# Performance work log

Measured on AMD Instinct MI355X. Metric: run time of the kernel, lower is better.

## Reference

```python
import jax, jax.numpy as jnp
import numpy as np

B, T, C = 4, 2048, 1024
H = 16
DH = C // H  # 64


def setup_inputs() -> dict:
    key = jax.random.key(0)
    ks = jax.random.split(key, 6)
    s = 1.0 / np.sqrt(C)
    x = jax.random.normal(ks[0], (B, T, C), dtype=jnp.float32)
    # per-head projection weights, stacked: (H, C, DH)
    Wq = jax.random.uniform(ks[1], (H, C, DH), dtype=jnp.float32, minval=-s, maxval=s)
    Wk = jax.random.uniform(ks[2], (H, C, DH), dtype=jnp.float32, minval=-s, maxval=s)
    Wv = jax.random.uniform(ks[3], (H, C, DH), dtype=jnp.float32, minval=-s, maxval=s)
    # output projection (torch Linear: y = x @ W.T + b); store as (C, C) for x @ Wo
    Wo = jax.random.uniform(ks[4], (C, C), dtype=jnp.float32, minval=-s, maxval=s)
    bo = jax.random.uniform(ks[5], (C,), dtype=jnp.float32, minval=-s, maxval=s)
    return {"x": x, "Wq": Wq, "Wk": Wk, "Wv": Wv, "Wo": Wo, "bo": bo}


def reference(x, Wq, Wk, Wv, Wo, bo):
    # x: (B,T,C) -> q,k,v: (B,H,T,DH)
    q = jnp.einsum('btc,hcd->bhtd', x, Wq)
    k = jnp.einsum('btc,hcd->bhtd', x, Wk)
    v = jnp.einsum('btc,hcd->bhtd', x, Wv)
    scale = DH ** -0.5
    scores = jnp.einsum('bhtd,bhsd->bhts', q, k) * scale  # (B,H,T,T)
    causal = jnp.tril(jnp.ones((T, T), dtype=bool))
    scores = jnp.where(causal, scores, -jnp.inf)
    wei = jax.nn.softmax(scores, axis=-1)
    out = jnp.einsum('bhts,bhsd->bhtd', wei, v)  # (B,H,T,DH)
    # concat heads: (B,T,H*DH) = (B,T,C)
    out = out.transpose(0, 2, 1, 3).reshape(B, T, C)
    return out @ Wo + bo
```

## Files before the change

kernel.cpp:

```cpp
#include <hip/hip_runtime.h>

#define T_SEQ 2048
#define C_DIM 1024
#define H_NUM 16
#define DHD   64
#define B_NUM 4
#define M_ROWS (B_NUM*T_SEQ)

typedef __bf16 bf16x8 __attribute__((ext_vector_type(8)));
typedef float  f32x4  __attribute__((ext_vector_type(4)));
typedef unsigned short ushort8 __attribute__((ext_vector_type(8)));
typedef unsigned short ushort4e __attribute__((ext_vector_type(4)));

__device__ __forceinline__ unsigned short f2b(float f){
  return __builtin_bit_cast(unsigned short, (__bf16)f);
}
__device__ __forceinline__ bf16x8 as_bf(ushort8 u){ return __builtin_bit_cast(bf16x8, u); }
__device__ __forceinline__ float exp2fast(float x){ return __builtin_amdgcn_exp2f(x); }

__device__ __forceinline__ void gload16(const void* g, void* l){
  __builtin_amdgcn_global_load_lds(
      (const __attribute__((address_space(1))) void*)g,
      (__attribute__((address_space(3))) void*)l, 16, 0, 0);
}

#define MF(a,b,c) __builtin_amdgcn_mfma_f32_16x16x32_bf16(a,b,c,0,0,0)

__global__ __launch_bounds__(256) void k_prep(const float* __restrict__ x,
                                              const float* __restrict__ wq,
                                              const float* __restrict__ wk,
                                              const float* __restrict__ wv,
                                              const float* __restrict__ wo,
                                              unsigned short* __restrict__ xb,
                                              unsigned short* __restrict__ wt,
                                              unsigned short* __restrict__ wot){
  const int bid = blockIdx.x;
  const int tid = threadIdx.x;
  if (bid < 8192){
    int i = bid*256 + tid;
    float4 f = ((const float4*)x)[i];
    ushort4e o;
    o[0]=f2b(f.x); o[1]=f2b(f.y); o[2]=f2b(f.z); o[3]=f2b(f.w);
    ((ushort4e*)xb)[i] = o;
    return;
  }
  __shared__ __align__(16) unsigned short vr[64][72];
  const int tb = bid - 8192;
  const float* S; int LS; unsigned short* D; int R0, C0; float scale = 1.f;
  if (tb < 768){
    int m = tb >> 8, rem = tb & 255;
    int h = rem >> 4, c0 = rem & 15;
    S = ((m==0)?wq:(m==1)?wk:wv) + (size_t)(h*16 + c0)*64*64;
    LS = 64;
    D = wt; R0 = m*1024 + h*64; C0 = c0*64;
    if (m == 0) scale = 0.125f * 1.4426950408889634f;
  } else {
    int tb2 = tb - 768;
    int nb = tb2 >> 4, cb = tb2 & 15;
    S = wo + (size_t)(cb*64)*1024 + nb*64;
    LS = 1024;
    D = wot; R0 = nb*64; C0 = cb*64;
  }
  #pragma unroll
  for (int i = 0; i < 2; i++){
    int id2 = tid + i*256;
    int r = id2 >> 3, e8 = (id2 & 7)*8;
    float4 a = *(const float4*)&S[(size_t)r*LS + e8];
    float4 b2 = *(const float4*)&S[(size_t)r*LS + e8 + 4];
    ushort8 u;
    u[0]=f2b(a.x*scale); u[1]=f2b(a.y*scale); u[2]=f2b(a.z*scale); u[3]=f2b(a.w*scale);
    u[4]=f2b(b2.x*scale); u[5]=f2b(b2.y*scale); u[6]=f2b(b2.z*scale); u[7]=f2b(b2.w*scale);
    *(ushort8*)&vr[r][e8 ^ ((r >> 3) << 3)] = u;
  }
  __syncthreads();
  #pragma unroll
  for (int i = 0; i < 2; i++){
    int id2 = tid + i*256;
    int d = id2 >> 3, oc = id2 & 7;
    ushort8 u;
    #pragma unroll
    for (int j = 0; j < 8; j++)
      u[j] = vr[oc*8 + j][d ^ (oc << 3)];
    *(ushort8*)&D[(size_t)(R0 + d)*1024 + C0 + oc*8] = u;
  }
}

__global__ __launch_bounds__(256) void k_gemm_qkv(const unsigned short* __restrict__ xb,
                                                  const unsigned short* __restrict__ wt,
                                                  unsigned short* __restrict__ qo,
                                                  unsigned short* __restrict__ ko,
                                                  unsigned short* __restrict__ vtr){
  __shared__ __align__(16) unsigned short smem[2][128*64];
  const int tid = threadIdx.x, lane = tid & 63, wid = tid >> 6;
  const int g = lane >> 4, tl = lane & 15;
  const int wr = wid >> 1, wc = wid & 1;
  const int id = blockIdx.x;
  const int xcd = id & 7, i = id >> 3;
  const int xm = xcd >> 1, xn = xcd & 1;
  const int mbase = (xm*16 + i/12) * 128, nbase = (xn*12 + i%12) * 128;
  const int sel = nbase >> 10;
  f32x4 acc[4][4] = {};
  if (sel < 2){
    for (int kk = 0; kk < C_DIM; kk += 64){
      __syncthreads();
      #pragma unroll
      for (int i2 = 0; i2 < 4; i2++){
        const int brow = (wid*4 + i2)*8;
        const int row  = brow + (lane >> 3);
        const int jj   = (lane & 7) ^ (row & 7);
        gload16(&xb[(size_t)(mbase+row)*C_DIM + kk + jj*8], &smem[0][brow*64]);
        gload16(&wt[(size_t)(nbase+row)*C_DIM + kk + jj*8], &smem[1][brow*64]);
      }
      __syncthreads();
      bf16x8 aF[4][2], bF[4][2];
      #pragma unroll
      for (int mb = 0; mb < 4; mb++){
        const int row = wr*64 + mb*16 + tl; const int s7 = row & 7;
        aF[mb][0] = as_bf(*(const ushort8*)&smem[0][row*64 + ((g     ^ s7)*8)]);
        aF[mb][1] = as_bf(*(const ushort8*)&smem[0][row*64 + (((4+g) ^ s7)*8)]);
      }
      #pragma unroll
      for (int nb = 0; nb < 4; nb++){
        const int row = wc*64 + nb*16 + tl; const int s7 = row & 7;
        bF[nb][0] = as_bf(*(const ushort8*)&smem[1][row*64 + ((g     ^ s7)*8)]);
        bF[nb][1] = as_bf(*(const ushort8*)&smem[1][row*64 + (((4+g) ^ s7)*8)]);
      }
      #pragma unroll
      for (int mb = 0; mb < 4; mb++)
        #pragma unroll
        for (int nb = 0; nb < 4; nb++){
          acc[mb][nb] = MF(bF[nb][0], aF[mb][0], acc[mb][nb]);
          acc[mb][nb] = MF(bF[nb][1], aF[mb][1], acc[mb][nb]);
        }
    }
    unsigned short* dst0 = (sel == 0) ? qo : ko;
    const int nloc = (nbase & 1023) + wc*64;
    #pragma unroll
    for (int mb = 0; mb < 4; mb++){
      const int t = mbase + wr*64 + mb*16 + tl;
      const int b = t >> 11, tt = t & 2047;
      #pragma unroll
      for (int nb = 0; nb < 4; nb++){
        const int nw = nloc + nb*16 + g*4;
        const int h = nw >> 6, d0 = nw & 63;
        ushort4e pk;
        #pragma unroll
        for (int r = 0; r < 4; r++) pk[r] = f2b(acc[mb][nb][r]);
        *(ushort4e*)&dst0[(((size_t)(b*H_NUM + h))*T_SEQ + tt)*DHD + d0] = pk;
      }
    }
  } else {
    for (int kk = 0; kk < C_DIM; kk += 64){
      __syncthreads();
      #pragma unroll
      for (int i2 = 0; i2 < 4; i2++){
        const int brow = (wid*4 + i2)*8;
        const int row  = brow + (lane >> 3);
        const int jj   = (lane & 7) ^ (row & 7);
        gload16(&xb[(size_t)(mbase+row)*C_DIM + kk + jj*8], &smem[0][brow*64]);
        gload16(&wt[(size_t)(nbase+row)*C_DIM + kk + jj*8], &smem[1][brow*64]);
      }
      __syncthreads();
      bf16x8 aF[4][2], bF[4][2];
      #pragma unroll
      for (int mb = 0; mb < 4; mb++){
        const int row = wr*64 + mb*16 + tl; const int s7 = row & 7;
        aF[mb][0] = as_bf(*(const ushort8*)&smem[0][row*64 + ((g     ^ s7)*8)]);
        aF[mb][1] = as_bf(*(const ushort8*)&smem[0][row*64 + (((4+g) ^ s7)*8)]);
      }
      #pragma unroll
      for (int nb = 0; nb < 4; nb++){
        const int row = wc*64 + nb*16 + tl; const int s7 = row & 7;
        bF[nb][0] = as_bf(*(const ushort8*)&smem[1][row*64 + ((g     ^ s7)*8)]);
        bF[nb][1] = as_bf(*(const ushort8*)&smem[1][row*64 + (((4+g) ^ s7)*8)]);
      }
      #pragma unroll
      for (int mb = 0; mb < 4; mb++)
        #pragma unroll
        for (int nb = 0; nb < 4; nb++){
          acc[mb][nb] = MF(aF[mb][0], bF[nb][0], acc[mb][nb]);
          acc[mb][nb] = MF(aF[mb][1], bF[nb][1], acc[mb][nb]);
        }
    }
    __syncthreads();
    unsigned short* tr = &smem[0][0];
    #pragma unroll
    for (int mb = 0; mb < 4; mb++){
      #pragma unroll
      for (int nb = 0; nb < 4; nb++){
        const int n = wc*64 + nb*16 + tl;
        const int m0 = wr*64 + mb*16 + g*4;
        ushort4e pk;
        #pragma unroll
        for (int r = 0; r < 4; r++) pk[r] = f2b(acc[mb][nb][r]);
        *(ushort4e*)&tr[n*128 + (m0 ^ ((n & 15) << 3))] = pk;
      }
    }
    __syncthreads();
    const int hbase = (nbase - 2048) >> 6;
    const int b = mbase >> 11, tloc = mbase & 2047;
    const int n = tid >> 1, half = tid & 1;
    unsigned short* vdst = vtr + (((size_t)(b*H_NUM + hbase + (n >> 6)))*DHD + (n & 63))*T_SEQ
                           + tloc + half*64;
    const int nx = (n & 15) << 3;
    #pragma unroll
    for (int c8 = 0; c8 < 8; c8++){
      const int t0 = half*64 + (c8 >> 2)*32 + (c8 & 3)*4;
      ushort4e lo = *(const ushort4e*)&tr[n*128 + ((t0     ) ^ nx)];
      ushort4e hi = *(const ushort4e*)&tr[n*128 + ((t0 + 16) ^ nx)];
      ushort8 u;
      #pragma unroll
      for (int e = 0; e < 4; e++){ u[e] = lo[e]; u[4+e] = hi[e]; }
      *(ushort8*)&vdst[c8*8] = u;
    }
  }
}

__global__ __launch_bounds__(512) void k_flash(const unsigned short* __restrict__ q,
                                               const unsigned short* __restrict__ k,
                                               const unsigned short* __restrict__ vtg,
                                               unsigned short* __restrict__ o){
  __shared__ __align__(16) unsigned short kbufs[2][128*64];
  __shared__ __align__(16) unsigned short vbufs[2][64*128];
  const int tid = threadIdx.x, lane = tid & 63, w = tid >> 6;
  const int g = lane >> 4, tl = lane & 15;
  const int id = blockIdx.x;
  const int kslot = id >> 3;
  const int bh = (id & 7)*8 + (kslot & 7);
  const int qsel = kslot >> 3;
  const int qt = (qsel < 4) ? qsel : (11 - qsel);
  const int b = bh >> 4, h = bh & 15;
  const unsigned short* qb = q   + (size_t)bh * T_SEQ * DHD;
  const unsigned short* kb = k   + (size_t)bh * T_SEQ * DHD;
  const unsigned short* vb = vtg + (size_t)bh * (size_t)DHD * T_SEQ;
  const int lrow = lane >> 3, lj = lane & 7;
  const int s7 = tl & 7;
  const int vre = lane >> 4;
  const int vh  = (lane >> 3) & 1;
  const int vcc = lane & 7;

  const int tbase = qt * 256;
  const int trow0 = tbase + w * 32;
  const int tmax = trow0 + 31;
  bf16x8 qF[2][2];
  #pragma unroll
  for (int tf = 0; tf < 2; tf++)
    #pragma unroll
    for (int ks = 0; ks < 2; ks++)
      qF[tf][ks] = as_bf(*(const ushort8*)&qb[(size_t)(trow0 + tf*16 + tl)*DHD + ks*32 + g*8]);
  f32x4 acc[2][4] = {};
  float mreg[2] = {-1e30f, -1e30f}, lreg[2] = {0.f, 0.f};
  const int nkt = 2*qt + 2;
  #pragma unroll
  for (int i = 0; i < 2; i++){
    const int krow = i*64 + w*8 + lrow;
    const int kjj  = lj ^ (krow & 7);
    gload16(&kb[(size_t)krow*DHD + kjj*8], &kbufs[0][(i*64 + w*8)*64]);
    const int vrow = i*32 + w*4 + vre;
    const int vjj  = vcc ^ (vrow & 7);
    gload16(&vb[(size_t)vrow*T_SEQ + vh*64 + vjj*8], &vbufs[0][(i*32 + w*4)*128]);
  }
  __syncthreads();
  for (int kti = 0; kti < nkt; ++kti){
    const int cur = kti & 1;
    const int kbase = kti * 128;
    if (kti + 1 < nkt){
      const int kb2 = kbase + 128;
      #pragma unroll
      for (int i = 0; i < 2; i++){
        const int krow = i*64 + w*8 + lrow;
        const int kjj  = lj ^ (krow & 7);
        gload16(&kb[(size_t)(kb2+krow)*DHD + kjj*8], &kbufs[cur^1][(i*64 + w*8)*64]);
        const int vrow = i*32 + w*4 + vre;
        const int vjj  = vcc ^ (vrow & 7);
        gload16(&vb[(size_t)vrow*T_SEQ + kb2 + vh*64 + vjj*8], &vbufs[cur^1][(i*32 + w*4)*128]);
      }
    }
    if (kbase <= tmax){
      const unsigned short* kcur = kbufs[cur];
      const unsigned short* vcur = vbufs[cur];
      f32x4 st[2][8] = {};
      __builtin_amdgcn_s_setprio(1);
      #pragma unroll
      for (int sf = 0; sf < 8; sf++){
        const int row = sf*16 + tl;
        const int r7 = row & 7;
        bf16x8 kf0 = as_bf(*(const ushort8*)&kcur[row*64 + ((g     ^ r7)*8)]);
        bf16x8 kf1 = as_bf(*(const ushort8*)&kcur[row*64 + (((4+g) ^ r7)*8)]);
        #pragma unroll
        for (int tf = 0; tf < 2; tf++){
          st[tf][sf] = MF(kf0, qF[tf][0], st[tf][sf]);
          st[tf][sf] = MF(kf1, qF[tf][1], st[tf][sf]);
        }
      }
      __builtin_amdgcn_s_setprio(0);
      if (kbase + 127 > trow0){
        #pragma unroll
        for (int tf = 0; tf < 2; tf++){
          int tg = trow0 + tf*16 + tl;
          #pragma unroll
          for (int sf = 0; sf < 8; sf++)
            #pragma unroll
            for (int r = 0; r < 4; r++)
              if (kbase + sf*16 + g*4 + r > tg) st[tf][sf][r] = -1e30f;
        }
      }
      bf16x8 pa[2][4];
      #pragma unroll
      for (int tf = 0; tf < 2; tf++){
        float mloc = -1e30f;
        #pragma unroll
        for (int sf = 0; sf < 8; sf++)
          #pragma unroll
          for (int r = 0; r < 4; r++) mloc = fmaxf(mloc, st[tf][sf][r]);
        if (__any(mloc > mreg[tf] + 8.f)){
          float mrow = fmaxf(mloc, __shfl_xor(mloc, 16));
          mrow = fmaxf(mrow, __shfl_xor(mrow, 32));
          float mnew = fmaxf(mreg[tf], mrow);
          float alpha = exp2fast(mreg[tf] - mnew);
          mreg[tf] = mnew;
          lreg[tf] *= alpha;
          #pragma unroll
          for (int df = 0; df < 4; df++)
            #pragma unroll
            for (int r = 0; r < 4; r++) acc[tf][df][r] *= alpha;
        }
        float sum = 0.f;
        #pragma unroll
        for (int q4 = 0; q4 < 4; q4++){
          ushort8 uu;
          #pragma unroll
          for (int r = 0; r < 4; r++){
            float p0 = exp2fast(st[tf][2*q4  ][r] - mreg[tf]);
            float p1 = exp2fast(st[tf][2*q4+1][r] - mreg[tf]);
            sum += p0 + p1;
            uu[r]   = f2b(p0);
            uu[4+r] = f2b(p1);
          }
          pa[tf][q4] = as_bf(uu);
        }
        lreg[tf] += sum;
      }
      __builtin_amdgcn_s_setprio(1);
      #pragma unroll
      for (int df = 0; df < 4; df++){
        const int row = df*16 + tl;
        bf16x8 vfr[4];
        #pragma unroll
        for (int q4 = 0; q4 < 4; q4++)
          vfr[q4] = as_bf(*(const ushort8*)&vcur[row*128 + (q4 >> 1)*64 + (((4*(q4 & 1) + g) ^ s7)*8)]);
        #pragma unroll
        for (int tf = 0; tf < 2; tf++)
          #pragma unroll
          for (int q4 = 0; q4 < 4; q4++)
            acc[tf][df] = MF(vfr[q4], pa[tf][q4], acc[tf][df]);
      }
      __builtin_amdgcn_s_setprio(0);
    }
    __syncthreads();
  }
  #pragma unroll
  for (int tf = 0; tf < 2; tf++){
    float l = lreg[tf];
    l += __shfl_xor(l, 16);
    l += __shfl_xor(l, 32);
    float inv = 1.f / l;
    int tg = trow0 + tf*16 + tl;
    #pragma unroll
    for (int df = 0; df < 4; df++){
      ushort4e ov;
      #pragma unroll
      for (int r = 0; r < 4; r++) ov[r] = f2b(acc[tf][df][r] * inv);
      *(ushort4e*)&o[((size_t)(b*T_SEQ + tg))*C_DIM + h*DHD + df*16 + g*4] = ov;
    }
  }
}

__global__ __launch_bounds__(256) void k_gemm_proj(const unsigned short* __restrict__ ab,
                                                   const unsigned short* __restrict__ wot,
                                                   const float* __restrict__ bo,
                                                   float* __restrict__ out){
  __shared__ __align__(16) unsigned short a_lds[128*64];
  __shared__ __align__(16) unsigned short b_lds[128*64];
  const int tid = threadIdx.x, lane = tid & 63, wid = tid >> 6;
  const int g = lane >> 4, tl = lane & 15;
  const int wr = wid >> 1, wc = wid & 1;
  const int id = blockIdx.x;
  const int swz = (id & 7)*64 + (id >> 3);
  const int mbase = (swz >> 3) * 128, nbase = (swz & 7) * 128;
  f32x4 acc[4][4] = {};
  for (int kk = 0; kk < C_DIM; kk += 64){
    __syncthreads();
    #pragma unroll
    for (int i = 0; i < 4; i++){
      const int brow = (wid*4 + i)*8;
      const int row  = brow + (lane >> 3);
      const int jj   = (lane & 7) ^ (row & 7);
      gload16(&ab[(size_t)(mbase+row)*C_DIM + kk + jj*8],  &a_lds[brow*64]);
      gload16(&wot[(size_t)(nbase+row)*C_DIM + kk + jj*8], &b_lds[brow*64]);
    }
    __syncthreads();
    bf16x8 aF[4][2], bF[4][2];
    #pragma unroll
    for (int mb = 0; mb < 4; mb++){
      const int row = wr*64 + mb*16 + tl; const int s7 = row & 7;
      aF[mb][0] = as_bf(*(const ushort8*)&a_lds[row*64 + ((g     ^ s7)*8)]);
      aF[mb][1] = as_bf(*(const ushort8*)&a_lds[row*64 + (((4+g) ^ s7)*8)]);
    }
    #pragma unroll
    for (int nb = 0; nb < 4; nb++){
      const int row = wc*64 + nb*16 + tl; const int s7 = row & 7;
      bF[nb][0] = as_bf(*(const ushort8*)&b_lds[row*64 + ((g     ^ s7)*8)]);
      bF[nb][1] = as_bf(*(const ushort8*)&b_lds[row*64 + (((4+g) ^ s7)*8)]);
    }
    #pragma unroll
    for (int mb = 0; mb < 4; mb++)
      #pragma unroll
      for (int nb = 0; nb < 4; nb++){
        acc[mb][nb] = MF(aF[mb][0], bF[nb][0], acc[mb][nb]);
        acc[mb][nb] = MF(aF[mb][1], bF[nb][1], acc[mb][nb]);
      }
  }
  #pragma unroll
  for (int mb = 0; mb < 4; mb++){
    #pragma unroll
    for (int nb = 0; nb < 4; nb++){
      #pragma unroll
      for (int r = 0; r < 4; r++){
        int gr = mbase + wr*64 + mb*16 + g*4 + r;
        int gc = nbase + wc*64 + nb*16 + tl;
        out[(size_t)gr*C_DIM + gc] = acc[mb][nb][r] + bo[gc];
      }
    }
  }
}

extern "C" void kernel_launch(void* const* d_in, const int* in_sizes, int n_in,
                              void* d_out, int out_size, void* d_ws, size_t ws_size,
                              hipStream_t stream){
  const float* x  = (const float*)d_in[0];
  const float* Wq = (const float*)d_in[1];
  const float* Wk = (const float*)d_in[2];
  const float* Wv = (const float*)d_in[3];
  const float* Wo = (const float*)d_in[4];
  const float* bo = (const float*)d_in[5];
  float* out = (float*)d_out;

  char* p = (char*)d_ws;
  unsigned short* xb  = (unsigned short*)p; p += (size_t)M_ROWS*C_DIM*2;
  unsigned short* wt  = (unsigned short*)p; p += (size_t)3*C_DIM*C_DIM*2;
  unsigned short* wot = (unsigned short*)p; p += (size_t)C_DIM*C_DIM*2;
  unsigned short* Qb  = (unsigned short*)p; p += (size_t)M_ROWS*C_DIM*2;
  unsigned short* Kb  = (unsigned short*)p; p += (size_t)M_ROWS*C_DIM*2;
  unsigned short* Vtr = (unsigned short*)p; p += (size_t)M_ROWS*C_DIM*2;
  unsigned short* attn = xb;

  hipLaunchKernelGGL(k_prep, dim3(8192 + 1024), dim3(256), 0, stream,
                     x, Wq, Wk, Wv, Wo, xb, wt, wot);
  hipLaunchKernelGGL(k_gemm_qkv, dim3(1536), dim3(256), 0, stream,
                     xb, wt, Qb, Kb, Vtr);
  hipLaunchKernelGGL(k_flash, dim3(512), dim3(512), 0, stream,
                     Qb, Kb, Vtr, attn);
  hipLaunchKernelGGL(k_gemm_proj, dim3(512), dim3(256), 0, stream,
                     attn, wot, bo, out);
}
```

Before: 163.7 us.

## Pair causal query tiles per block and stage 256-row K/V chunks

The flash attention kernel now launches 256 blocks, each processing two query tiles (bx and 7-bx) one after another, which balances causal work across blocks. K/V staging grows from 128 to 256 keys per double-buffered stage, and each stage is consumed in two 128-key halves, so the number of barriers and load rounds drops by half. LDS usage doubles to 128 KB per block, which limits occupancy to one block per CU. The sequential two-pass loop may also leave CUs idle with only 256 blocks on the device.

```diff
diff --git a/kernel.cpp b/kernel.cpp
--- a/kernel.cpp
+++ b/kernel.cpp
@@ -220,158 +220,157 @@
                                                const unsigned short* __restrict__ k,
                                                const unsigned short* __restrict__ vtg,
                                                unsigned short* __restrict__ o){
-  __shared__ __align__(16) unsigned short kbufs[2][128*64];
-  __shared__ __align__(16) unsigned short vbufs[2][64*128];
+  __shared__ __align__(16) unsigned short kbufs[2][256*64];
+  __shared__ __align__(16) unsigned short vbufs[2][64*256];
   const int tid = threadIdx.x, lane = tid & 63, w = tid >> 6;
   const int g = lane >> 4, tl = lane & 15;
   const int id = blockIdx.x;
-  const int kslot = id >> 3;
-  const int bh = (id & 7)*8 + (kslot & 7);
-  const int qsel = kslot >> 3;
-  const int qt = (qsel < 4) ? qsel : (11 - qsel);
+  const int swz = (id & 7)*32 + (id >> 3);
+  const int bh = swz >> 2, bx = swz & 3;
   const int b = bh >> 4, h = bh & 15;
   const unsigned short* qb = q   + (size_t)bh * T_SEQ * DHD;
   const unsigned short* kb = k   + (size_t)bh * T_SEQ * DHD;
   const unsigned short* vb = vtg + (size_t)bh * (size_t)DHD * T_SEQ;
   const int lrow = lane >> 3, lj = lane & 7;
   const int s7 = tl & 7;
-  const int vre = lane >> 4;
-  const int vh  = (lane >> 3) & 1;
-  const int vcc = lane & 7;
-
-  const int tbase = qt * 256;
-  const int trow0 = tbase + w * 32;
-  const int tmax = trow0 + 31;
-  bf16x8 qF[2][2];
-  #pragma unroll
-  for (int tf = 0; tf < 2; tf++)
-    #pragma unroll
-    for (int ks = 0; ks < 2; ks++)
-      qF[tf][ks] = as_bf(*(const ushort8*)&qb[(size_t)(trow0 + tf*16 + tl)*DHD + ks*32 + g*8]);
-  f32x4 acc[2][4] = {};
-  float mreg[2] = {-1e30f, -1e30f}, lreg[2] = {0.f, 0.f};
-  const int nkt = 2*qt + 2;
-  #pragma unroll
-  for (int i = 0; i < 2; i++){
-    const int krow = i*64 + w*8 + lrow;
-    const int kjj  = lj ^ (krow & 7);
-    gload16(&kb[(size_t)krow*DHD + kjj*8], &kbufs[0][(i*64 + w*8)*64]);
-    const int vrow = i*32 + w*4 + vre;
-    const int vjj  = vcc ^ (vrow & 7);
-    gload16(&vb[(size_t)vrow*T_SEQ + vh*64 + vjj*8], &vbufs[0][(i*32 + w*4)*128]);
-  }
-  __syncthreads();
-  for (int kti = 0; kti < nkt; ++kti){
-    const int cur = kti & 1;
-    const int kbase = kti * 128;
-    if (kti + 1 < nkt){
-      const int kb2 = kbase + 128;
-      #pragma unroll
-      for (int i = 0; i < 2; i++){
-        const int krow = i*64 + w*8 + lrow;
-        const int kjj  = lj ^ (krow & 7);
-        gload16(&kb[(size_t)(kb2+krow)*DHD + kjj*8], &kbufs[cur^1][(i*64 + w*8)*64]);
-        const int vrow = i*32 + w*4 + vre;
-        const int vjj  = vcc ^ (vrow & 7);
-        gload16(&vb[(size_t)vrow*T_SEQ + kb2 + vh*64 + vjj*8], &vbufs[cur^1][(i*32 + w*4)*128]);
-      }
-    }
-    if (kbase <= tmax){
-      const unsigned short* kcur = kbufs[cur];
-      const unsigned short* vcur = vbufs[cur];
-      f32x4 st[2][8] = {};
-      __builtin_amdgcn_s_setprio(1);
-      #pragma unroll
-      for (int sf = 0; sf < 8; sf++){
-        const int row = sf*16 + tl;
-        const int r7 = row & 7;
-        bf16x8 kf0 = as_bf(*(const ushort8*)&kcur[row*64 + ((g     ^ r7)*8)]);
-        bf16x8 kf1 = as_bf(*(const ushort8*)&kcur[row*64 + (((4+g) ^ r7)*8)]);
-        #pragma unroll
-        for (int tf = 0; tf < 2; tf++){
-          st[tf][sf] = MF(kf0, qF[tf][0], st[tf][sf]);
-          st[tf][sf] = MF(kf1, qF[tf][1], st[tf][sf]);
+  const int vq = (lane >> 3) & 3;
+
+  for (int pass = 0; pass < 2; ++pass){
+    const int qt = pass ? (7 - bx) : bx;
+    const int tbase = qt * 256;
+    const int trow0 = tbase + w * 32;
+    const int tmax = trow0 + 31;
+    bf16x8 qF[2][2];
+    #pragma unroll
+    for (int tf = 0; tf < 2; tf++)
+      #pragma unroll
+      for (int ks = 0; ks < 2; ks++)
+        qF[tf][ks] = as_bf(*(const ushort8*)&qb[(size_t)(trow0 + tf*16 + tl)*DHD + ks*32 + g*8]);
+    f32x4 acc[2][4] = {};
+    float mreg[2] = {-1e30f, -1e30f}, lreg[2] = {0.f, 0.f};
+    const int nkt = qt + 1;
+    #pragma unroll
+    for (int i = 0; i < 4; i++){
+      const int krow = i*64 + w*8 + lrow;
+      gload16(&kb[(size_t)krow*DHD + ((lj ^ (krow & 7))*8)], &kbufs[0][(i*64 + w*8)*64]);
+      const int vrow = i*16 + w*2 + (lane >> 5);
+      gload16(&vb[(size_t)vrow*T_SEQ + vq*64 + ((lj ^ (vrow & 7))*8)], &vbufs[0][(i*16 + w*2)*256]);
+    }
+    __syncthreads();
+    for (int kti = 0; kti < nkt; ++kti){
+      const int cur = kti & 1;
+      const int kb256 = kti * 256;
+      if (kti + 1 < nkt){
+        const int kb2 = kb256 + 256;
+        #pragma unroll
+        for (int i = 0; i < 4; i++){
+          const int krow = i*64 + w*8 + lrow;
+          gload16(&kb[(size_t)(kb2+krow)*DHD + ((lj ^ (krow & 7))*8)], &kbufs[cur^1][(i*64 + w*8)*64]);
+          const int vrow = i*16 + w*2 + (lane >> 5);
+          gload16(&vb[(size_t)vrow*T_SEQ + kb2 + vq*64 + ((lj ^ (vrow & 7))*8)], &vbufs[cur^1][(i*16 + w*2)*256]);
         }
       }
-      __builtin_amdgcn_s_setprio(0);
-      if (kbase + 127 > trow0){
-        #pragma unroll
-        for (int tf = 0; tf < 2; tf++){
-          int tg = trow0 + tf*16 + tl;
+      #pragma unroll
+      for (int sh = 0; sh < 2; sh++){
+        const int kbase = kb256 + sh*128;
+        if (kbase <= tmax){
+          const unsigned short* kcur = &kbufs[cur][sh*128*64];
+          const unsigned short* vcur = &vbufs[cur][0];
+          f32x4 st[2][8] = {};
+          __builtin_amdgcn_s_setprio(1);
           #pragma unroll
-          for (int sf = 0; sf < 8; sf++)
-            #pragma unroll
-            for (int r = 0; r < 4; r++)
-              if (kbase + sf*16 + g*4 + r > tg) st[tf][sf][r] = -1e30f;
+          for (int sf = 0; sf < 8; sf++){
+            const int row = sf*16 + tl;
+            const int r7 = row & 7;
+            bf16x8 kf0 = as_bf(*(const ushort8*)&kcur[row*64 + ((g     ^ r7)*8)]);
+            bf16x8 kf1 = as_bf(*(const ushort8*)&kcur[row*64 + (((4+g) ^ r7)*8)]);
+            #pragma unroll
+            for (int tf = 0; tf < 2; tf++){
+              st[tf][sf] = MF(kf0, qF[tf][0], st[tf][sf]);
+              st[tf][sf] = MF(kf1, qF[tf][1], st[tf][sf]);
+            }
+          }
+          __builtin_amdgcn_s_setprio(0);
+          if (kbase + 127 > trow0){
+            #pragma unroll
+            for (int tf = 0; tf < 2; tf++){
+              int tg = trow0 + tf*16 + tl;
+              #pragma unroll
+              for (int sf = 0; sf < 8; sf++)
+                #pragma unroll
+                for (int r = 0; r < 4; r++)
+                  if (kbase + sf*16 + g*4 + r > tg) st[tf][sf][r] = -1e30f;
+            }
+          }
+          bf16x8 pa[2][4];
+          #pragma unroll
+          for (int tf = 0; tf < 2; tf++){
+            float mloc = -1e30f;
+            #pragma unroll
+            for (int sf = 0; sf < 8; sf++)
+              #pragma unroll
+              for (int r = 0; r < 4; r++) mloc = fmaxf(mloc, st[tf][sf][r]);
+            if (__any(mloc > mreg[tf] + 8.f)){
+              float mrow = fmaxf(mloc, __shfl_xor(mloc, 16));
+              mrow = fmaxf(mrow, __shfl_xor(mrow, 32));
+              float mnew = fmaxf(mreg[tf], mrow);
+              float alpha = exp2fast(mreg[tf] - mnew);
+              mreg[tf] = mnew;
+              lreg[tf] *= alpha;
+              #pragma unroll
+              for (int df = 0; df < 4; df++)
+                #pragma unroll
+                for (int r = 0; r < 4; r++) acc[tf][df][r] *= alpha;
+            }
+            float sum = 0.f;
+            #pragma unroll
+            for (int q4 = 0; q4 < 4; q4++){
+              ushort8 uu;
+              #pragma unroll
+              for (int r = 0; r < 4; r++){
+                float p0 = exp2fast(st[tf][2*q4  ][r] - mreg[tf]);
+                float p1 = exp2fast(st[tf][2*q4+1][r] - mreg[tf]);
+                sum += p0 + p1;
+                uu[r]   = f2b(p0);
+                uu[4+r] = f2b(p1);
+              }
+              pa[tf][q4] = as_bf(uu);
+            }
+            lreg[tf] += sum;
+          }
+          __builtin_amdgcn_s_setprio(1);
+          #pragma unroll
+          for (int df = 0; df < 4; df++){
+            const int row = df*16 + tl;
+            bf16x8 vfr[4];
+            #pragma unroll
+            for (int q4 = 0; q4 < 4; q4++)
+              vfr[q4] = as_bf(*(const ushort8*)&vcur[row*256 + sh*128 + (q4 >> 1)*64 + (((4*(q4 & 1) + g) ^ s7)*8)]);
+            #pragma unroll
+            for (int tf = 0; tf < 2; tf++)
+              #pragma unroll
+              for (int q4 = 0; q4 < 4; q4++)
+                acc[tf][df] = MF(vfr[q4], pa[tf][q4], acc[tf][df]);
+          }
+          __builtin_amdgcn_s_setprio(0);
         }
       }
-      bf16x8 pa[2][4];
-      #pragma unroll
-      for (int tf = 0; tf < 2; tf++){
-        float mloc = -1e30f;
-        #pragma unroll
-        for (int sf = 0; sf < 8; sf++)
-          #pragma unroll
-          for (int r = 0; r < 4; r++) mloc = fmaxf(mloc, st[tf][sf][r]);
-        if (__any(mloc > mreg[tf] + 8.f)){
-          float mrow = fmaxf(mloc, __shfl_xor(mloc, 16));
-          mrow = fmaxf(mrow, __shfl_xor(mrow, 32));
-          float mnew = fmaxf(mreg[tf], mrow);
-          float alpha = exp2fast(mreg[tf] - mnew);
-          mreg[tf] = mnew;
-          lreg[tf] *= alpha;
-          #pragma unroll
-          for (int df = 0; df < 4; df++)
-            #pragma unroll
-            for (int r = 0; r < 4; r++) acc[tf][df][r] *= alpha;
-        }
-        float sum = 0.f;
-        #pragma unroll
-        for (int q4 = 0; q4 < 4; q4++){
-          ushort8 uu;
-          #pragma unroll
-          for (int r = 0; r < 4; r++){
-            float p0 = exp2fast(st[tf][2*q4  ][r] - mreg[tf]);
-            float p1 = exp2fast(st[tf][2*q4+1][r] - mreg[tf]);
-            sum += p0 + p1;
-            uu[r]   = f2b(p0);
-            uu[4+r] = f2b(p1);
-          }
-          pa[tf][q4] = as_bf(uu);
-        }
-        lreg[tf] += sum;
-      }
-      __builtin_amdgcn_s_setprio(1);
+      __syncthreads();
+    }
+    #pragma unroll
+    for (int tf = 0; tf < 2; tf++){
+      float l = lreg[tf];
+      l += __shfl_xor(l, 16);
+      l += __shfl_xor(l, 32);
+      float inv = 1.f / l;
+      int tg = trow0 + tf*16 + tl;
       #pragma unroll
       for (int df = 0; df < 4; df++){
-        const int row = df*16 + tl;
-        bf16x8 vfr[4];
-        #pragma unroll
-        for (int q4 = 0; q4 < 4; q4++)
-          vfr[q4] = as_bf(*(const ushort8*)&vcur[row*128 + (q4 >> 1)*64 + (((4*(q4 & 1) + g) ^ s7)*8)]);
-        #pragma unroll
-        for (int tf = 0; tf < 2; tf++)
-          #pragma unroll
-          for (int q4 = 0; q4 < 4; q4++)
-            acc[tf][df] = MF(vfr[q4], pa[tf][q4], acc[tf][df]);
-      }
-      __builtin_amdgcn_s_setprio(0);
-    }
-    __syncthreads();
-  }
-  #pragma unroll
-  for (int tf = 0; tf < 2; tf++){
-    float l = lreg[tf];
-    l += __shfl_xor(l, 16);
-    l += __shfl_xor(l, 32);
-    float inv = 1.f / l;
-    int tg = trow0 + tf*16 + tl;
-    #pragma unroll
-    for (int df = 0; df < 4; df++){
-      ushort4e ov;
-      #pragma unroll
-      for (int r = 0; r < 4; r++) ov[r] = f2b(acc[tf][df][r] * inv);
-      *(ushort4e*)&o[((size_t)(b*T_SEQ + tg))*C_DIM + h*DHD + df*16 + g*4] = ov;
+        ushort4e ov;
+        #pragma unroll
+        for (int r = 0; r < 4; r++) ov[r] = f2b(acc[tf][df][r] * inv);
+        *(ushort4e*)&o[((size_t)(b*T_SEQ + tg))*C_DIM + h*DHD + df*16 + g*4] = ov;
+      }
     }
   }
 }
@@ -459,7 +458,7 @@
                      x, Wq, Wk, Wv, Wo, xb, wt, wot);
   hipLaunchKernelGGL(k_gemm_qkv, dim3(1536), dim3(256), 0, stream,
                      xb, wt, Qb, Kb, Vtr);
-  hipLaunchKernelGGL(k_flash, dim3(512), dim3(512), 0, stream,
+  hipLaunchKernelGGL(k_flash, dim3(256), dim3(512), 0, stream,
                      Qb, Kb, Vtr, attn);
   hipLaunchKernelGGL(k_gemm_proj, dim3(512), dim3(256), 0, stream,
                      attn, wot, bo, out);
```

After: 163.0 us. No clear change (-0.4%).
